# Optimization experiments

Hardware: AMD Instinct MI355X
Metric: run time of the kernel (lower is better)

The kernel has to match this reference:

```python
import jax, jax.numpy as jnp
import numpy as np

B, S, HID = 4, 2048, 1024
NH, IM, E = 4, 2048, 4
EPS = 1e-6


def setup_inputs() -> dict:
    key = jax.random.key(0)
    ks = jax.random.split(key, 12)
    init = lambda k, shape: (jax.random.normal(k, shape, jnp.float32) * 0.02)
    return {
        "hidden_states": jax.random.normal(ks[0], (B, S, HID), jnp.float32),
        "ln1_w": jnp.ones((HID,), jnp.float32),
        "wq": init(ks[1], (HID, HID)),
        "wk": init(ks[2], (HID, HID)),
        "wv": init(ks[3], (HID, HID)),
        "wo": init(ks[4], (HID, HID)),
        "ln2_w": jnp.ones((HID,), jnp.float32),
        "router_w": init(ks[5], (HID, E)),
        "router_b": jnp.zeros((E,), jnp.float32),
        "gate_w": init(ks[6], (E, HID, IM)),
        "up_w": init(ks[7], (E, HID, IM)),
        "down_w": init(ks[8], (E, IM, HID)),
    }


def _rms(x, w):
    return w * (x * jax.lax.rsqrt(jnp.mean(x * x, axis=-1, keepdims=True) + EPS))


def reference(hidden_states, ln1_w, wq, wk, wv, wo, ln2_w,
              router_w, router_b, gate_w, up_w, down_w):
    b, s, h = hidden_states.shape
    nh, d = NH, h // NH

    # ---- attention block (elu+1 feature map, then full softmax) ----
    x = _rms(hidden_states, ln1_w)
    q = (x @ wq).reshape(b, s, nh, d).transpose(0, 2, 1, 3)  # [b,nh,s,d]
    k = (x @ wk).reshape(b, s, nh, d).transpose(0, 2, 1, 3)
    v = (x @ wv).reshape(b, s, nh, d).transpose(0, 2, 1, 3)
    q = jax.nn.elu(q) + 1.0
    k = jax.nn.elu(k) + 1.0
    scores = jnp.einsum('bhqd,bhkd->bhqk', q, k)
    attn = jax.nn.softmax(scores, axis=-1)  # dropout is identity at eval
    o = jnp.einsum('bhqk,bhkd->bhqd', attn, v)
    o = o.transpose(0, 2, 1, 3).reshape(b, s, h) @ wo
    h1 = hidden_states + o

    # ---- MoE block: router softmax, balance loss, dense expert loop ----
    x2 = _rms(h1, ln2_w)
    logits = x2 @ router_w + router_b            # [b,s,E]
    rw = jax.nn.softmax(logits, axis=-1)
    mean_routing = rw.mean(axis=0)               # mean over batch dim only, [s,E]
    balance_loss = jnp.mean((mean_routing - 1.0 / E) ** 2) * 0.01

    # source computes EVERY expert over all tokens, weighted by the FULL
    # softmax routing weight (top-k weights are computed but unused)
    moe_out = jnp.zeros_like(x2)
    for i in range(E):
        g = jax.nn.silu(x2 @ gate_w[i])
        u = x2 @ up_w[i]
        moe_out = moe_out + ((g * u) @ down_w[i]) * rw[..., i:i + 1]

    return h1 + moe_out, balance_loss
```

## Files before the change

### kernel.cpp

```cpp
#include <hip/hip_runtime.h>
#include <cstdint>
#include <cstddef>

#define B_    4
#define S_    2048
#define HID_  1024
#define NH_   4
#define HD_   256
#define IM_   2048
#define E_    4
#define M_    8192
#define NHG_  4

typedef __bf16 bf16x8 __attribute__((ext_vector_type(8)));
typedef float  f32x4  __attribute__((ext_vector_type(4)));

__device__ __forceinline__ unsigned short f32_to_bf16(float f) {
  unsigned int u = __float_as_uint(f);
  u += 0x7fffu + ((u >> 16) & 1u);
  return (unsigned short)(u >> 16);
}

__device__ __forceinline__ void gload16(const unsigned short* g, unsigned short* l) {
  __builtin_amdgcn_global_load_lds(
      (const __attribute__((address_space(1))) void*)g,
      (__attribute__((address_space(3))) void*)l, 16, 0, 0);
}

__device__ __forceinline__ void swizzle_xy(int& bx, int& by) {
  const int gx = gridDim.x, gy = gridDim.y;
  const int flat = blockIdx.x + blockIdx.y * gx;
  const int xcd = flat & 7, i = flat >> 3;
  const int rpx = gy >> 3;
  bx = i % gx;
  by = xcd * rpx + i / gx;
}

#define EPI_F32      0
#define EPI_VT       2
#define EPI_PV_O     3
#define EPI_WO       4
#define EPI_DOWN     5

struct EpiAux {
  float* c_f32;
  unsigned short* c_bf16;
  const float* add_src;
  float* out2;
  long long strideCz;
  int ldc;
};

template<int EPI>
__global__ __launch_bounds__(256) void gemm_bf16k(
    const unsigned short* __restrict__ A, int lda, long long sAo, long long sAi, int zbA,
    const unsigned short* __restrict__ B, int ldb, long long sBo, long long sBi, int zbB,
    int zshift, int zmask, int zbC, int K, EpiAux aux)
{
  __shared__ unsigned short As[2][128 * 32];
  __shared__ unsigned short Bs[2][128 * 32];

  const int t = threadIdx.x;
  int bx, by;
  swizzle_xy(bx, by);
  const int m0 = by * 128, n0 = bx * 128;
  const int z  = blockIdx.z;
  const int zA = z + zbA, zB = z + zbB, zC = z + zbC;
  const unsigned short* Ab = A + (long long)(zA >> zshift) * sAo + (long long)(zA & zmask) * sAi;
  const unsigned short* Bb = B + (long long)(zB >> zshift) * sBo + (long long)(zB & zmask) * sBi;

  const int lane = t & 63, wave = t >> 6;
  const int wm = (wave >> 1) * 64, wn = (wave & 1) * 64;
  const int lrow = lane & 15, quad = lane >> 4;

  f32x4 acc[4][4] = {};

  const int srow = lane >> 2;
  const int sko  = (lane & 3) * 8;
  const unsigned short* aRow0 = Ab + (long long)(m0 + wave * 16       + srow) * lda + sko;
  const unsigned short* aRow1 = Ab + (long long)(m0 + (wave + 4) * 16 + srow) * lda + sko;
  const unsigned short* bRow0 = Bb + (long long)(n0 + wave * 16       + srow) * ldb + sko;
  const unsigned short* bRow1 = Bb + (long long)(n0 + (wave + 4) * 16 + srow) * ldb + sko;
  const int dst0 = (wave * 16) * 32, dst1 = ((wave + 4) * 16) * 32;

  gload16(aRow0, &As[0][dst0]);
  gload16(aRow1, &As[0][dst1]);
  gload16(bRow0, &Bs[0][dst0]);
  gload16(bRow1, &Bs[0][dst1]);

  int cur = 0;
  for (int kk = 0; kk < K; kk += 32, cur ^= 1) {
    __syncthreads();
    if (kk + 32 < K) {
      const int nxt = cur ^ 1, k2 = kk + 32;
      gload16(aRow0 + k2, &As[nxt][dst0]);
      gload16(aRow1 + k2, &As[nxt][dst1]);
      gload16(bRow0 + k2, &Bs[nxt][dst0]);
      gload16(bRow1 + k2, &Bs[nxt][dst1]);
    }
    bf16x8 af[4], bfr[4];
    #pragma unroll
    for (int i = 0; i < 4; ++i) {
      af[i]  = *reinterpret_cast<const bf16x8*>(&As[cur][(wm + i * 16 + lrow) * 32 + quad * 8]);
      bfr[i] = *reinterpret_cast<const bf16x8*>(&Bs[cur][(wn + i * 16 + lrow) * 32 + quad * 8]);
    }
    #pragma unroll
    for (int i = 0; i < 4; ++i)
      #pragma unroll
      for (int j = 0; j < 4; ++j)
        acc[i][j] = __builtin_amdgcn_mfma_f32_16x16x32_bf16(af[i], bfr[j], acc[i][j], 0, 0, 0);
  }

  #pragma unroll
  for (int mi = 0; mi < 4; ++mi) {
    #pragma unroll
    for (int ni = 0; ni < 4; ++ni) {
      #pragma unroll
      for (int r = 0; r < 4; ++r) {
        const int gm = m0 + wm + mi * 16 + quad * 4 + r;
        const int gn = n0 + wn + ni * 16 + lrow;
        const float val = acc[mi][ni][r];
        if (EPI == EPI_F32) {
          aux.c_f32[(long long)zC * aux.strideCz + (long long)gm * aux.ldc + gn] = val;
        } else if (EPI == EPI_VT) {
          const int b = gm >> 11, s = gm & (S_ - 1);
          const int h = gn >> 8, d = gn & (HD_ - 1);
          aux.c_bf16[((long long)(b * NH_ + h) * HD_ + d) * S_ + s] = f32_to_bf16(val);
        } else if (EPI == EPI_PV_O) {
          const int b = zC >> 2, h = zC & (NH_ - 1);
          aux.c_bf16[((long long)(b * S_ + gm)) * HID_ + h * HD_ + gn] = f32_to_bf16(val);
        } else if (EPI == EPI_WO) {
          const long long idx = (long long)gm * HID_ + gn;
          aux.out2[idx] = val + aux.add_src[idx];
        } else if (EPI == EPI_DOWN) {
          const long long idx = (long long)gm * HID_ + gn;
          aux.out2[idx] += val;
        }
      }
    }
  }
}

#define EPI2_GU 1

template<int EPI2>
__global__ __launch_bounds__(256, 2) void gemm_dual_k(
    const unsigned short* __restrict__ A,
    const unsigned short* __restrict__ B0b,
    const unsigned short* __restrict__ B1b,
    int zb,
    unsigned short* __restrict__ out0, unsigned short* __restrict__ out1,
    const float* __restrict__ rw)
{
  __shared__ unsigned short As[2][128 * 32];
  __shared__ unsigned short B0s[2][128 * 32];
  __shared__ unsigned short B1s[2][128 * 32];

  const int t = threadIdx.x;
  int bx, by;
  swizzle_xy(bx, by);
  const int m0 = by * 128, n0 = bx * 128;

  const int lane = t & 63, wave = t >> 6;
  const int wm = (wave >> 1) * 64, wn = (wave & 1) * 64;
  const int lrow = lane & 15, quad = lane >> 4;

  f32x4 acc0[4][4] = {}, acc1[4][4] = {};

  const int srow = lane >> 2;
  const int sko  = (lane & 3) * 8;
  const unsigned short* aRow0 = A   + (long long)(m0 + wave * 16       + srow) * HID_ + sko;
  const unsigned short* aRow1 = A   + (long long)(m0 + (wave + 4) * 16 + srow) * HID_ + sko;
  const unsigned short* gRow0 = B0b + (long long)(n0 + wave * 16       + srow) * HID_ + sko;
  const unsigned short* gRow1 = B0b + (long long)(n0 + (wave + 4) * 16 + srow) * HID_ + sko;
  const unsigned short* uRow0 = B1b + (long long)(n0 + wave * 16       + srow) * HID_ + sko;
  const unsigned short* uRow1 = B1b + (long long)(n0 + (wave + 4) * 16 + srow) * HID_ + sko;
  const int dst0 = (wave * 16) * 32, dst1 = ((wave + 4) * 16) * 32;

  gload16(aRow0, &As[0][dst0]);
  gload16(aRow1, &As[0][dst1]);
  gload16(gRow0, &B0s[0][dst0]);
  gload16(gRow1, &B0s[0][dst1]);
  gload16(uRow0, &B1s[0][dst0]);
  gload16(uRow1, &B1s[0][dst1]);

  int cur = 0;
  for (int kk = 0; kk < HID_; kk += 32, cur ^= 1) {
    __syncthreads();
    if (kk + 32 < HID_) {
      const int nxt = cur ^ 1, k2 = kk + 32;
      gload16(aRow0 + k2, &As[nxt][dst0]);
      gload16(aRow1 + k2, &As[nxt][dst1]);
      gload16(gRow0 + k2, &B0s[nxt][dst0]);
      gload16(gRow1 + k2, &B0s[nxt][dst1]);
      gload16(uRow0 + k2, &B1s[nxt][dst0]);
      gload16(uRow1 + k2, &B1s[nxt][dst1]);
    }
    bf16x8 af[4], b0[4], b1[4];
    #pragma unroll
    for (int i = 0; i < 4; ++i) {
      af[i] = *reinterpret_cast<const bf16x8*>(&As[cur][(wm + i * 16 + lrow) * 32 + quad * 8]);
      b0[i] = *reinterpret_cast<const bf16x8*>(&B0s[cur][(wn + i * 16 + lrow) * 32 + quad * 8]);
      b1[i] = *reinterpret_cast<const bf16x8*>(&B1s[cur][(wn + i * 16 + lrow) * 32 + quad * 8]);
    }
    #pragma unroll
    for (int i = 0; i < 4; ++i)
      #pragma unroll
      for (int j = 0; j < 4; ++j) {
        acc0[i][j] = __builtin_amdgcn_mfma_f32_16x16x32_bf16(af[i], b0[j], acc0[i][j], 0, 0, 0);
        acc1[i][j] = __builtin_amdgcn_mfma_f32_16x16x32_bf16(af[i], b1[j], acc1[i][j], 0, 0, 0);
      }
  }

  #pragma unroll
  for (int mi = 0; mi < 4; ++mi)
    #pragma unroll
    for (int r = 0; r < 4; ++r) {
      const int gm = m0 + wm + mi * 16 + quad * 4 + r;
      const float rwv = rw[(long long)gm * E_ + zb];
      #pragma unroll
      for (int ni = 0; ni < 4; ++ni) {
        const int gn = n0 + wn + ni * 16 + lrow;
        const float v0 = acc0[mi][ni][r];
        const float v1 = acc1[mi][ni][r];
        const float sg = v0 / (1.f + __expf(-v0));
        out0[(long long)gm * IM_ + gn] = f32_to_bf16(sg * v1 * rwv);
      }
    }
}

#define EPI4_GU   0
#define EPI4_QK   1
#define EPI4_DOWN 2
template<bool DUAL, int EPI, int KTOT, int KROW, bool PAIRK>
__global__ __launch_bounds__(512, 2) void gemm4p_k(
    const unsigned short* A0, const unsigned short* A1,
    const unsigned short* B0b, const unsigned short* B1b,
    const float* __restrict__ rw, int expert,
    unsigned short* out0, unsigned short* out1, float* o_f32)
{
  constexpr int NT  = KTOT / 64;
  constexpr int NT2 = NT / 2;
  __shared__ unsigned short smem[DUAL ? 65536 : 49152];

  const int t = threadIdx.x, wave = t >> 6, lane = t & 63;
  const int lrow = lane & 15, quad = lane >> 4;
  const int wrow0 = (wave >> 1) * 64;
  const int wcol0 = (wave & 1) * 64;

  int bx, by;
  swizzle_xy(bx, by);
  const int m0 = by * 256, n0 = bx * 128;

  const int r8  = lane >> 3;
  const int csw = ((lane & 7) ^ r8) << 4;

  auto stage_unit = [&](const unsigned short* mat, int grow0, int ktl, int ldsElem) {
    #pragma unroll
    for (int i = 0; i < 2; ++i) {
      const char* src = (const char*)(mat + (size_t)(grow0 + wave * 16 + i * 8 + r8) * KROW)
                        + (size_t)ktl * 128 + csw;
      gload16((const unsigned short*)src, &smem[ldsElem + wave * 1024 + i * 512]);
    }
  };
  auto stageA = [&](int kt, int buf) {
    const unsigned short* m = A0; int ktl = kt;
    if (PAIRK && kt >= NT2) { m = A1; ktl = kt - NT2; }
    stage_unit(m, m0,       ktl, buf * 16384);
    stage_unit(m, m0 + 128, ktl, buf * 16384 + 8192);
  };
  auto stageB = [&](int kt, int buf, int which) {
    const unsigned short* m; int ktl = kt; int base;
    if (PAIRK) {
      if (kt >= NT2) { m = B1b; ktl = kt - NT2; } else { m = B0b; }
      base = 32768;
    } else {
      m = which ? B1b : B0b;
      base = which ? 49152 : 32768;
    }
    stage_unit(m, n0, ktl, base + buf * 8192);
  };

  const int xr = (lane & 7) << 4;
  auto readA_ = [&](bf16x8* o, int buf, int ks) {
    const char* base = (const char*)smem + buf * 32768 + (wrow0 >> 7) * 16384;
    const int rl0 = wrow0 & 64;
    #pragma unroll
    for (int mi = 0; mi < 4; ++mi)
      o[mi] = *(const bf16x8*)(base + (rl0 + mi * 16 + lrow) * 128 + ((ks * 64 + quad * 16) ^ xr));
  };
  auto readB_ = [&](bf16x8* o, int buf, int which, int ks) {
    const char* base = (const char*)smem + (which ? 98304 : 65536) + buf * 16384;
    #pragma unroll
    for (int nj = 0; nj < 4; ++nj)
      o[nj] = *(const bf16x8*)(base + (wcol0 + nj * 16 + lrow) * 128 + ((ks * 64 + quad * 16) ^ xr));
  };

  f32x4 acc0[4][4] = {};
  f32x4 acc1[4][4] = {};
  auto mm = [&](f32x4 (&ac)[4][4], const bf16x8* aF, const bf16x8* bF) {
    #pragma unroll
    for (int mi = 0; mi < 4; ++mi)
      #pragma unroll
      for (int nj = 0; nj < 4; ++nj)
        ac[mi][nj] = __builtin_amdgcn_mfma_f32_16x16x32_bf16(aF[mi], bF[nj], ac[mi][nj], 0, 0, 0);
  };

  stageA(0, 0);
  stageB(0, 0, 0);
  if (DUAL) stageB(0, 0, 1);
  stageA(1, 1);
  asm volatile("s_waitcnt vmcnt(4)" ::: "memory");
  __builtin_amdgcn_s_barrier();

  bf16x8 a0[4], a1[4], bF[4];
  for (int T = 0; T < NT; ++T) {
    const int c = T & 1;
    if (DUAL) {
      readA_(a0, c, 0); readB_(bF, c, 0, 0);
      if (T + 1 < NT) stageB(T + 1, c ^ 1, 0);
      __builtin_amdgcn_s_barrier();
      asm volatile("s_waitcnt lgkmcnt(0)" ::: "memory");
      __builtin_amdgcn_s_setprio(1); mm(acc0, a0, bF); __builtin_amdgcn_s_setprio(0);
      __builtin_amdgcn_s_barrier();
      readB_(bF, c, 1, 0);
      if (T + 1 < NT) stageB(T + 1, c ^ 1, 1);
      __builtin_amdgcn_s_barrier();
      asm volatile("s_waitcnt lgkmcnt(0)" ::: "memory");
      __builtin_amdgcn_s_setprio(1); mm(acc1, a0, bF); __builtin_amdgcn_s_setprio(0);
      __builtin_amdgcn_s_barrier();
      readA_(a1, c, 1); readB_(bF, c, 0, 1);
      __builtin_amdgcn_s_barrier();
      asm volatile("s_waitcnt lgkmcnt(0)" ::: "memory");
      __builtin_amdgcn_s_setprio(1); mm(acc0, a1, bF); __builtin_amdgcn_s_setprio(0);
      __builtin_amdgcn_s_barrier();
      readB_(bF, c, 1, 1);
      if (T + 2 < NT) { stageA(T + 2, c); asm volatile("s_waitcnt vmcnt(4)" ::: "memory"); }
      else            { asm volatile("s_waitcnt vmcnt(0)" ::: "memory"); }
      __builtin_amdgcn_s_barrier();
      asm volatile("s_waitcnt lgkmcnt(0)" ::: "memory");
      __builtin_amdgcn_s_setprio(1); mm(acc1, a1, bF); __builtin_amdgcn_s_setprio(0);
      __builtin_amdgcn_s_barrier();
    } else {
      readA_(a0, c, 0); readA_(a1, c, 1); readB_(bF, c, 0, 0);
      if (T + 1 < NT) stageB(T + 1, c ^ 1, 0);
      __builtin_amdgcn_s_barrier();
      asm volatile("s_waitcnt lgkmcnt(0)" ::: "memory");
      __builtin_amdgcn_s_setprio(1); mm(acc0, a0, bF); __builtin_amdgcn_s_setprio(0);
      __builtin_amdgcn_s_barrier();
      readB_(bF, c, 0, 1);
      if (T + 2 < NT) { stageA(T + 2, c); asm volatile("s_waitcnt vmcnt(4)" ::: "memory"); }
      else            { asm volatile("s_waitcnt vmcnt(0)" ::: "memory"); }
      __builtin_amdgcn_s_barrier();
      asm volatile("s_waitcnt lgkmcnt(0)" ::: "memory");
      __builtin_amdgcn_s_setprio(1); mm(acc0, a1, bF); __builtin_amdgcn_s_setprio(0);
      __builtin_amdgcn_s_barrier();
    }
  }

  #pragma unroll
  for (int mi = 0; mi < 4; ++mi) {
    #pragma unroll
    for (int r = 0; r < 4; ++r) {
      const int gm = m0 + wrow0 + mi * 16 + quad * 4 + r;
      float rwv = 0.f;
      if (EPI == EPI4_GU) rwv = rw[(size_t)gm * E_ + expert];
      #pragma unroll
      for (int nj = 0; nj < 4; ++nj) {
        const int gn = n0 + wcol0 + nj * 16 + lrow;
        const float v0 = acc0[mi][nj][r];
        if (EPI == EPI4_GU) {
          const float v1 = acc1[mi][nj][r];
          const float sg = v0 / (1.f + __expf(-v0));
          out0[(size_t)gm * IM_ + gn] = f32_to_bf16(sg * v1 * rwv);
        } else if (EPI == EPI4_QK) {
          const float v1 = acc1[mi][nj][r];
          out0[(size_t)gm * HID_ + gn] = f32_to_bf16(v0 > 0.f ? v0 + 1.f : __expf(v0));
          out1[(size_t)gm * HID_ + gn] = f32_to_bf16(v1 > 0.f ? v1 + 1.f : __expf(v1));
        } else {
          o_f32[(size_t)gm * HID_ + gn] += v0;
        }
      }
    }
  }
}

__global__ void transpose_cast4_k(const float* s0, const float* s1,
                                  const float* s2, const float* s3,
                                  unsigned short* __restrict__ out, int R, int C)
{
  __shared__ float tile[32][33];
  const int z = blockIdx.z;
  const float* in = (z == 0) ? s0 : (z == 1) ? s1 : (z == 2) ? s2 : s3;
  unsigned short* o = out + (long long)z * R * C;
  const int c0 = blockIdx.x * 32, r0 = blockIdx.y * 32;
  const int tx = threadIdx.x, ty = threadIdx.y;
  #pragma unroll
  for (int i = 0; i < 32; i += 8)
    tile[ty + i][tx] = in[(long long)(r0 + ty + i) * C + c0 + tx];
  __syncthreads();
  #pragma unroll
  for (int i = 0; i < 32; i += 8)
    o[(long long)(c0 + ty + i) * R + r0 + tx] = f32_to_bf16(tile[tx][ty + i]);
}

__global__ void transpose_cast2x4_k(const float* __restrict__ sA,
                                    const float* __restrict__ sB,
                                    unsigned short* __restrict__ dA,
                                    unsigned short* __restrict__ dB,
                                    int R, int C)
{
  __shared__ float tile[32][33];
  const int z = blockIdx.z;
  const long long eo = (long long)(z & 3) * R * C;
  const float* in = ((z < 4) ? sA : sB) + eo;
  unsigned short* o = ((z < 4) ? dA : dB) + eo;
  const int c0 = blockIdx.x * 32, r0 = blockIdx.y * 32;
  const int tx = threadIdx.x, ty = threadIdx.y;
  #pragma unroll
  for (int i = 0; i < 32; i += 8)
    tile[ty + i][tx] = in[(long long)(r0 + ty + i) * C + c0 + tx];
  __syncthreads();
  #pragma unroll
  for (int i = 0; i < 32; i += 8)
    o[(long long)(c0 + ty + i) * R + r0 + tx] = f32_to_bf16(tile[tx][ty + i]);
}

__global__ void transpose_cast_k(const float* __restrict__ in,
                                 unsigned short* __restrict__ out, int R, int C)
{
  __shared__ float tile[32][33];
  const long long bo = (long long)blockIdx.z * R * C;
  const int c0 = blockIdx.x * 32, r0 = blockIdx.y * 32;
  const int tx = threadIdx.x, ty = threadIdx.y;
  #pragma unroll
  for (int i = 0; i < 32; i += 8)
    tile[ty + i][tx] = in[bo + (long long)(r0 + ty + i) * C + c0 + tx];
  __syncthreads();
  #pragma unroll
  for (int i = 0; i < 32; i += 8)
    out[bo + (long long)(c0 + ty + i) * R + r0 + tx] = f32_to_bf16(tile[tx][ty + i]);
}

__global__ __launch_bounds__(256) void rmsnorm_cast_k(
    const float* __restrict__ x, const float* __restrict__ w,
    unsigned short* __restrict__ out)
{
  __shared__ float red[4];
  const int row = blockIdx.x, t = threadIdx.x;
  const float4 v = reinterpret_cast<const float4*>(x + (long long)row * HID_)[t];
  float ss = v.x * v.x + v.y * v.y + v.z * v.z + v.w * v.w;
  #pragma unroll
  for (int off = 32; off > 0; off >>= 1) ss += __shfl_down(ss, off, 64);
  if ((t & 63) == 0) red[t >> 6] = ss;
  __syncthreads();
  ss = red[0] + red[1] + red[2] + red[3];
  const float inv = rsqrtf(ss * (1.0f / HID_) + 1e-6f);
  const float4 wv = reinterpret_cast<const float4*>(w)[t];
  ushort4 o;
  o.x = f32_to_bf16(v.x * inv * wv.x);
  o.y = f32_to_bf16(v.y * inv * wv.y);
  o.z = f32_to_bf16(v.z * inv * wv.z);
  o.w = f32_to_bf16(v.w * inv * wv.w);
  reinterpret_cast<ushort4*>(out + (long long)row * HID_)[t] = o;
}

__global__ __launch_bounds__(256) void softmax_rows_k(float* __restrict__ scores)
{
  __shared__ float red[4];
  const long long rbase = ((long long)blockIdx.y * S_ + blockIdx.x) * S_;
  float* row = scores + rbase;
  const int t = threadIdx.x;
  float v[8];
  #pragma unroll
  for (int i = 0; i < 8; ++i) v[i] = row[t + i * 256];
  float m = v[0];
  #pragma unroll
  for (int i = 1; i < 8; ++i) m = fmaxf(m, v[i]);
  #pragma unroll
  for (int off = 32; off > 0; off >>= 1) m = fmaxf(m, __shfl_down(m, off, 64));
  if ((t & 63) == 0) red[t >> 6] = m;
  __syncthreads();
  m = fmaxf(fmaxf(red[0], red[1]), fmaxf(red[2], red[3]));
  __syncthreads();
  float s = 0.f;
  #pragma unroll
  for (int i = 0; i < 8; ++i) { v[i] = __expf(v[i] - m); s += v[i]; }
  #pragma unroll
  for (int off = 32; off > 0; off >>= 1) s += __shfl_down(s, off, 64);
  if ((t & 63) == 0) red[t >> 6] = s;
  __syncthreads();
  const float inv = 1.0f / (red[0] + red[1] + red[2] + red[3]);
  unsigned short* prow = reinterpret_cast<unsigned short*>(scores) + rbase * 2;
  #pragma unroll
  for (int i = 0; i < 8; ++i) prow[t + i * 256] = f32_to_bf16(v[i] * inv);
}

__global__ __launch_bounds__(256) void router_k(
    const float* __restrict__ h1, const float* __restrict__ ln2w,
    const float* __restrict__ rwgt, const float* __restrict__ rbias,
    float* __restrict__ rw)
{
  const int wv = threadIdx.x >> 6, lane = threadIdx.x & 63;
  const long long m = (long long)blockIdx.x * 4 + wv;
  const float* xr = h1 + m * HID_;
  float xv[16];
  float ss = 0.f;
  #pragma unroll
  for (int i = 0; i < 16; ++i) { xv[i] = xr[lane + i * 64]; ss += xv[i] * xv[i]; }
  #pragma unroll
  for (int off = 32; off > 0; off >>= 1) ss += __shfl_down(ss, off, 64);
  ss = __shfl(ss, 0, 64);
  const float inv = rsqrtf(ss * (1.0f / HID_) + 1e-6f);
  float l0 = 0, l1 = 0, l2 = 0, l3 = 0;
  #pragma unroll
  for (int i = 0; i < 16; ++i) {
    const int k = lane + i * 64;
    const float xn = xv[i] * inv * ln2w[k];
    const float4 wr = reinterpret_cast<const float4*>(rwgt)[k];
    l0 += xn * wr.x; l1 += xn * wr.y; l2 += xn * wr.z; l3 += xn * wr.w;
  }
  #pragma unroll
  for (int off = 32; off > 0; off >>= 1) {
    l0 += __shfl_down(l0, off, 64);
    l1 += __shfl_down(l1, off, 64);
    l2 += __shfl_down(l2, off, 64);
    l3 += __shfl_down(l3, off, 64);
  }
  if (lane == 0) {
    l0 += rbias[0]; l1 += rbias[1]; l2 += rbias[2]; l3 += rbias[3];
    const float mx = fmaxf(fmaxf(l0, l1), fmaxf(l2, l3));
    const float e0 = __expf(l0 - mx), e1 = __expf(l1 - mx);
    const float e2 = __expf(l2 - mx), e3 = __expf(l3 - mx);
    const float is = 1.0f / (e0 + e1 + e2 + e3);
    reinterpret_cast<float4*>(rw)[m] = make_float4(e0 * is, e1 * is, e2 * is, e3 * is);
  }
}

__global__ __launch_bounds__(256) void balance_k(const float* __restrict__ rw,
                                                 float* __restrict__ out_scalar)
{
  __shared__ float red[4];
  float acc = 0.f;
  for (int it = threadIdx.x; it < S_ * E_; it += 256) {
    const int s = it >> 2, e = it & 3;
    float mr = 0.f;
    #pragma unroll
    for (int b = 0; b < B_; ++b) mr += rw[((long long)b * S_ + s) * E_ + e];
    mr *= (1.0f / B_);
    const float d = mr - 1.0f / E_;
    acc += d * d;
  }
  #pragma unroll
  for (int off = 32; off > 0; off >>= 1) acc += __shfl_down(acc, off, 64);
  if ((threadIdx.x & 63) == 0) red[threadIdx.x >> 6] = acc;
  __syncthreads();
  if (threadIdx.x == 0)
    out_scalar[0] = (red[0] + red[1] + red[2] + red[3]) * (0.01f / (S_ * E_));
}

extern "C" void kernel_launch(void* const* d_in, const int* in_sizes, int n_in,
                              void* d_out, int out_size, void* d_ws, size_t ws_size,
                              hipStream_t stream)
{
  const float* hidden   = (const float*)d_in[0];
  const float* ln1w     = (const float*)d_in[1];
  const float* wq       = (const float*)d_in[2];
  const float* wk       = (const float*)d_in[3];
  const float* wv       = (const float*)d_in[4];
  const float* wo       = (const float*)d_in[5];
  const float* ln2w     = (const float*)d_in[6];
  const float* router_w = (const float*)d_in[7];
  const float* router_b = (const float*)d_in[8];
  const float* gate_w   = (const float*)d_in[9];
  const float* up_w     = (const float*)d_in[10];
  const float* down_w   = (const float*)d_in[11];
  float* out = (float*)d_out;

  char* ws = (char*)d_ws;
  size_t off = 0;
  auto carve = [&](size_t bytes) {
    off = (off + 255) & ~(size_t)255;
    char* p = ws + off;
    off += bytes;
    return p;
  };
  unsigned short* wqT   = (unsigned short*)carve((size_t)HID_ * HID_ * 2);
  unsigned short* wkT   = (unsigned short*)carve((size_t)HID_ * HID_ * 2);
  unsigned short* wvT   = (unsigned short*)carve((size_t)HID_ * HID_ * 2);
  unsigned short* woT   = (unsigned short*)carve((size_t)HID_ * HID_ * 2);
  unsigned short* x_bf  = (unsigned short*)carve((size_t)M_ * HID_ * 2);
  unsigned short* qb    = (unsigned short*)carve((size_t)M_ * HID_ * 2);
  unsigned short* kb    = (unsigned short*)carve((size_t)M_ * HID_ * 2);
  unsigned short* vT    = (unsigned short*)carve((size_t)M_ * HID_ * 2);
  float*          rwbuf = (float*)carve((size_t)M_ * E_ * 4);
  char*           ubase = carve((size_t)NHG_ * S_ * S_ * 4);
  float*          scores = (float*)ubase;
  unsigned short* gateT = (unsigned short*)(ubase);
  unsigned short* upT   = (unsigned short*)(ubase + (size_t)16 * 1024 * 1024);
  unsigned short* downT = (unsigned short*)(ubase + (size_t)32 * 1024 * 1024);
  unsigned short* o_bf  = x_bf;
  unsigned short* x2_bf = qb;
  unsigned short* gu0   = kb;
  unsigned short* gu1   = (unsigned short*)carve((size_t)M_ * IM_ * 2);
  const bool paired = (ws_size >= off);

  const dim3 blk256(256), blk512(512), blkT(32, 8);

  transpose_cast4_k<<<dim3(32, 32, 4), blkT, 0, stream>>>(wq, wk, wv, wo, wqT, HID_, HID_);

  rmsnorm_cast_k<<<M_, blk256, 0, stream>>>(hidden, ln1w, x_bf);

  gemm4p_k<true, EPI4_QK, 1024, 1024, false><<<dim3(8, 32, 1), blk512, 0, stream>>>(
      x_bf, nullptr, wqT, wkT, nullptr, 0, qb, kb, nullptr);
  {
    EpiAux a{}; a.c_bf16 = vT;
    gemm_bf16k<EPI_VT><<<dim3(8, 64, 1), blk256, 0, stream>>>(
        x_bf, HID_, 0, 0, 0, wvT, HID_, 0, 0, 0, 0, 0, 0, HID_, a);
  }

  for (int grp = 0; grp < 16 / NHG_; ++grp) {
    EpiAux as{}; as.c_f32 = scores; as.ldc = S_; as.strideCz = (long long)S_ * S_;
    gemm_bf16k<EPI_F32><<<dim3(16, 16, NHG_), blk256, 0, stream>>>(
        qb, HID_, (long long)S_ * HID_, HD_, grp * NHG_,
        kb, HID_, (long long)S_ * HID_, HD_, grp * NHG_,
        2, 3, 0, HD_, as);
    softmax_rows_k<<<dim3(S_, NHG_, 1), blk256, 0, stream>>>(scores);
    EpiAux ap{}; ap.c_bf16 = o_bf;
    gemm_bf16k<EPI_PV_O><<<dim3(2, 16, NHG_), blk256, 0, stream>>>(
        (const unsigned short*)scores, 2 * S_, (long long)S_ * 2 * S_, 0, 0,
        vT, S_, (long long)HD_ * S_, 0, grp * NHG_,
        0, 0, grp * NHG_, S_, ap);
  }

  transpose_cast2x4_k<<<dim3(64, 32, 8), blkT, 0, stream>>>(
      gate_w, up_w, gateT, upT, HID_, IM_);
  transpose_cast_k<<<dim3(32, 64, E_), blkT, 0, stream>>>(down_w, downT, IM_, HID_);

  {
    EpiAux a{}; a.add_src = hidden; a.out2 = out;
    gemm_bf16k<EPI_WO><<<dim3(8, 64, 1), blk256, 0, stream>>>(
        o_bf, HID_, 0, 0, 0, woT, HID_, 0, 0, 0, 0, 0, 0, HID_, a);
  }

  rmsnorm_cast_k<<<M_, blk256, 0, stream>>>(out, ln2w, x2_bf);
  router_k<<<M_ / 4, blk256, 0, stream>>>(out, ln2w, router_w, router_b, rwbuf);
  balance_k<<<1, blk256, 0, stream>>>(rwbuf, out + (size_t)M_ * HID_);

  const size_t wsz = (size_t)IM_ * HID_;
  if (paired) {
    for (int p = 0; p < 2; ++p) {
      const int e0 = 2 * p, e1 = e0 + 1;
      gemm4p_k<true, EPI4_GU, 1024, 1024, false><<<dim3(16, 32, 1), blk512, 0, stream>>>(
          x2_bf, nullptr, gateT + (size_t)e0 * wsz, upT + (size_t)e0 * wsz,
          rwbuf, e0, gu0, nullptr, nullptr);
      gemm4p_k<true, EPI4_GU, 1024, 1024, false><<<dim3(16, 32, 1), blk512, 0, stream>>>(
          x2_bf, nullptr, gateT + (size_t)e1 * wsz, upT + (size_t)e1 * wsz,
          rwbuf, e1, gu1, nullptr, nullptr);
      gemm4p_k<false, EPI4_DOWN, 4096, 2048, true><<<dim3(8, 32, 1), blk512, 0, stream>>>(
          gu0, gu1, downT + (size_t)e0 * wsz, downT + (size_t)e1 * wsz,
          nullptr, 0, nullptr, nullptr, out);
    }
  } else {
    for (int i = 0; i < E_; ++i) {
      gemm_dual_k<EPI2_GU><<<dim3(16, 64, 1), blk256, 0, stream>>>(
          x2_bf, gateT + (size_t)i * wsz, upT + (size_t)i * wsz, i, gu0, nullptr, rwbuf);
      EpiAux ad{}; ad.out2 = out;
      gemm_bf16k<EPI_DOWN><<<dim3(8, 64, 1), blk256, 0, stream>>>(
          gu0, IM_, 0, 0, 0, downT + (size_t)i * wsz, IM_, 0, 0, 0,
          0, 0, 0, IM_, ad);
    }
  }
}
```

Measured before the change: 1.070 ms.

## Deepen GEMM prefetch pipeline and route Wo projection through 512-thread GEMM

Restructures the 512-thread GEMM's load schedule. The dual-B path now prefetches the second B matrix two k-tiles ahead. The single-B path gets a three-slot B ring buffer so B is staged two tiles ahead, with vmcnt waits tuned so load latency overlaps more MFMA work. The Wo output projection with residual add moves from the older 256-thread GEMM to this kernel using a new epilogue. Shared memory for the non-dual variant grows, which may affect occupancy, and the hand-counted vmcnt values must stay correct to avoid races.

```diff
diff --git a/kernel.cpp b/kernel.cpp
--- a/kernel.cpp
+++ b/kernel.cpp
@@ -25,6 +25,16 @@
   __builtin_amdgcn_global_load_lds(
       (const __attribute__((address_space(1))) void*)g,
       (__attribute__((address_space(3))) void*)l, 16, 0, 0);
+}
+
+template<int N> __device__ __forceinline__ void vwait() {
+  if constexpr (N == 0)      asm volatile("s_waitcnt vmcnt(0)" ::: "memory");
+  else if constexpr (N == 2) asm volatile("s_waitcnt vmcnt(2)" ::: "memory");
+  else if constexpr (N == 6) asm volatile("s_waitcnt vmcnt(6)" ::: "memory");
+  else                       asm volatile("s_waitcnt vmcnt(8)" ::: "memory");
+}
+__device__ __forceinline__ void lgk0() {
+  asm volatile("s_waitcnt lgkmcnt(0)" ::: "memory");
 }
 
 __device__ __forceinline__ void swizzle_xy(int& bx, int& by) {
@@ -229,19 +239,21 @@
     }
 }
 
-#define EPI4_GU   0
-#define EPI4_QK   1
-#define EPI4_DOWN 2
+#define EPI5_GU   0
+#define EPI5_QK   1
+#define EPI5_DOWN 2
+#define EPI5_WO   3
 template<bool DUAL, int EPI, int KTOT, int KROW, bool PAIRK>
-__global__ __launch_bounds__(512, 2) void gemm4p_k(
+__global__ __launch_bounds__(512, 2) void gemm5_k(
     const unsigned short* A0, const unsigned short* A1,
     const unsigned short* B0b, const unsigned short* B1b,
     const float* __restrict__ rw, int expert,
-    unsigned short* out0, unsigned short* out1, float* o_f32)
+    unsigned short* out0, unsigned short* out1,
+    float* o_f32, const float* add_src)
 {
   constexpr int NT  = KTOT / 64;
   constexpr int NT2 = NT / 2;
-  __shared__ unsigned short smem[DUAL ? 65536 : 49152];
+  __shared__ unsigned short smem[DUAL ? 65536 : 57344];
 
   const int t = threadIdx.x, wave = t >> 6, lane = t & 63;
   const int lrow = lane & 15, quad = lane >> 4;
@@ -255,7 +267,7 @@
   const int r8  = lane >> 3;
   const int csw = ((lane & 7) ^ r8) << 4;
 
-  auto stage_unit = [&](const unsigned short* mat, int grow0, int ktl, int ldsElem) {
+  auto unit = [&](const unsigned short* mat, int grow0, int ktl, int ldsElem) {
     #pragma unroll
     for (int i = 0; i < 2; ++i) {
       const char* src = (const char*)(mat + (size_t)(grow0 + wave * 16 + i * 8 + r8) * KROW)
@@ -263,34 +275,34 @@
       gload16((const unsigned short*)src, &smem[ldsElem + wave * 1024 + i * 512]);
     }
   };
-  auto stageA = [&](int kt, int buf) {
+  auto stageA = [&](int kt) {
     const unsigned short* m = A0; int ktl = kt;
-    if (PAIRK && kt >= NT2) { m = A1; ktl = kt - NT2; }
-    stage_unit(m, m0,       ktl, buf * 16384);
-    stage_unit(m, m0 + 128, ktl, buf * 16384 + 8192);
+    if constexpr (PAIRK) { if (kt >= NT2) { m = A1; ktl = kt - NT2; } }
+    const int buf = kt & 1;
+    unit(m, m0,       ktl, buf * 16384);
+    unit(m, m0 + 128, ktl, buf * 16384 + 8192);
   };
-  auto stageB = [&](int kt, int buf, int which) {
-    const unsigned short* m; int ktl = kt; int base;
-    if (PAIRK) {
-      if (kt >= NT2) { m = B1b; ktl = kt - NT2; } else { m = B0b; }
-      base = 32768;
+  auto stageB = [&](int kt, int which, int bufB) {
+    const unsigned short* m; int ktl = kt;
+    if constexpr (DUAL) {
+      m = which ? B1b : B0b;
     } else {
-      m = which ? B1b : B0b;
-      base = which ? 49152 : 32768;
-    }
-    stage_unit(m, n0, ktl, base + buf * 8192);
+      m = B0b;
+      if constexpr (PAIRK) { if (kt >= NT2) { m = B1b; ktl = kt - NT2; } }
+    }
+    unit(m, n0, ktl, 32768 + (DUAL ? which * 16384 : 0) + bufB * 8192);
   };
 
   const int xr = (lane & 7) << 4;
   auto readA_ = [&](bf16x8* o, int buf, int ks) {
     const char* base = (const char*)smem + buf * 32768 + (wrow0 >> 7) * 16384;
-    const int rl0 = wrow0 & 64;
+    const int rl0 = wrow0 & 127;
     #pragma unroll
     for (int mi = 0; mi < 4; ++mi)
       o[mi] = *(const bf16x8*)(base + (rl0 + mi * 16 + lrow) * 128 + ((ks * 64 + quad * 16) ^ xr));
   };
-  auto readB_ = [&](bf16x8* o, int buf, int which, int ks) {
-    const char* base = (const char*)smem + (which ? 98304 : 65536) + buf * 16384;
+  auto readB_ = [&](bf16x8* o, int baseByte, int ks) {
+    const char* base = (const char*)smem + baseByte;
     #pragma unroll
     for (int nj = 0; nj < 4; ++nj)
       o[nj] = *(const bf16x8*)(base + (wcol0 + nj * 16 + lrow) * 128 + ((ks * 64 + quad * 16) ^ xr));
@@ -306,55 +318,72 @@
         ac[mi][nj] = __builtin_amdgcn_mfma_f32_16x16x32_bf16(aF[mi], bF[nj], ac[mi][nj], 0, 0, 0);
   };
 
-  stageA(0, 0);
-  stageB(0, 0, 0);
-  if (DUAL) stageB(0, 0, 1);
-  stageA(1, 1);
-  asm volatile("s_waitcnt vmcnt(4)" ::: "memory");
-  __builtin_amdgcn_s_barrier();
-
   bf16x8 a0[4], a1[4], bF[4];
-  for (int T = 0; T < NT; ++T) {
-    const int c = T & 1;
-    if (DUAL) {
-      readA_(a0, c, 0); readB_(bF, c, 0, 0);
-      if (T + 1 < NT) stageB(T + 1, c ^ 1, 0);
-      __builtin_amdgcn_s_barrier();
-      asm volatile("s_waitcnt lgkmcnt(0)" ::: "memory");
+
+  if constexpr (DUAL) {
+    stageA(0); stageB(0, 1, 0); stageB(0, 0, 0); stageA(1); stageB(1, 1, 1);
+    vwait<8>();
+    __builtin_amdgcn_s_barrier();
+
+    for (int T = 0; T < NT; ++T) {
+      const int c = T & 1;
+      const int bB1 = 65536 + 32768 + c * 16384;
+      const int bB0 = 65536 + c * 16384;
+      readA_(a0, c, 0);
+      readB_(bF, bB1, 0);
+      if (T + 1 < NT) stageB(T + 1, 0, (T + 1) & 1);
+      if (T < NT - 1) vwait<8>(); else vwait<0>();
+      __builtin_amdgcn_s_barrier();
+      lgk0();
+      __builtin_amdgcn_s_setprio(1); mm(acc1, a0, bF); __builtin_amdgcn_s_setprio(0);
+      __builtin_amdgcn_s_barrier();
+      readB_(bF, bB0, 0);
+      __builtin_amdgcn_s_barrier();
+      lgk0();
       __builtin_amdgcn_s_setprio(1); mm(acc0, a0, bF); __builtin_amdgcn_s_setprio(0);
       __builtin_amdgcn_s_barrier();
-      readB_(bF, c, 1, 0);
-      if (T + 1 < NT) stageB(T + 1, c ^ 1, 1);
-      __builtin_amdgcn_s_barrier();
-      asm volatile("s_waitcnt lgkmcnt(0)" ::: "memory");
-      __builtin_amdgcn_s_setprio(1); mm(acc1, a0, bF); __builtin_amdgcn_s_setprio(0);
-      __builtin_amdgcn_s_barrier();
-      readA_(a1, c, 1); readB_(bF, c, 0, 1);
-      __builtin_amdgcn_s_barrier();
-      asm volatile("s_waitcnt lgkmcnt(0)" ::: "memory");
+      readA_(a1, c, 1);
+      readB_(bF, bB1, 1);
+      __builtin_amdgcn_s_barrier();
+      lgk0();
+      __builtin_amdgcn_s_setprio(1); mm(acc1, a1, bF); __builtin_amdgcn_s_setprio(0);
+      __builtin_amdgcn_s_barrier();
+      readB_(bF, bB0, 1);
+      if (T + 2 < NT) { stageA(T + 2); stageB(T + 2, 1, c); }
+      if (T < NT - 2) vwait<8>();
+      else if (T == NT - 2) vwait<2>();
+      __builtin_amdgcn_s_barrier();
+      lgk0();
       __builtin_amdgcn_s_setprio(1); mm(acc0, a1, bF); __builtin_amdgcn_s_setprio(0);
       __builtin_amdgcn_s_barrier();
-      readB_(bF, c, 1, 1);
-      if (T + 2 < NT) { stageA(T + 2, c); asm volatile("s_waitcnt vmcnt(4)" ::: "memory"); }
-      else            { asm volatile("s_waitcnt vmcnt(0)" ::: "memory"); }
-      __builtin_amdgcn_s_barrier();
-      asm volatile("s_waitcnt lgkmcnt(0)" ::: "memory");
-      __builtin_amdgcn_s_setprio(1); mm(acc1, a1, bF); __builtin_amdgcn_s_setprio(0);
-      __builtin_amdgcn_s_barrier();
-    } else {
-      readA_(a0, c, 0); readA_(a1, c, 1); readB_(bF, c, 0, 0);
-      if (T + 1 < NT) stageB(T + 1, c ^ 1, 0);
-      __builtin_amdgcn_s_barrier();
-      asm volatile("s_waitcnt lgkmcnt(0)" ::: "memory");
+    }
+  } else {
+    stageB(0, 0, 0); stageA(0); stageB(1, 0, 1); stageA(1);
+    vwait<6>();
+    __builtin_amdgcn_s_barrier();
+
+    int b = 0;
+    for (int T = 0; T < NT; ++T) {
+      const int c = T & 1;
+      const int bB = 65536 + b * 16384;
+      int bn = b + 2; if (bn >= 3) bn -= 3;
+      readA_(a0, c, 0);
+      readA_(a1, c, 1);
+      readB_(bF, bB, 0);
+      if (T + 2 < NT) stageB(T + 2, 0, bn);
+      __builtin_amdgcn_s_barrier();
+      lgk0();
       __builtin_amdgcn_s_setprio(1); mm(acc0, a0, bF); __builtin_amdgcn_s_setprio(0);
       __builtin_amdgcn_s_barrier();
-      readB_(bF, c, 0, 1);
-      if (T + 2 < NT) { stageA(T + 2, c); asm volatile("s_waitcnt vmcnt(4)" ::: "memory"); }
-      else            { asm volatile("s_waitcnt vmcnt(0)" ::: "memory"); }
-      __builtin_amdgcn_s_barrier();
-      asm volatile("s_waitcnt lgkmcnt(0)" ::: "memory");
+      readB_(bF, bB, 1);
+      if (T + 2 < NT) stageA(T + 2);
+      if (T < NT - 2) vwait<6>();
+      else if (T == NT - 2) vwait<0>();
+      __builtin_amdgcn_s_barrier();
+      lgk0();
       __builtin_amdgcn_s_setprio(1); mm(acc0, a1, bF); __builtin_amdgcn_s_setprio(0);
       __builtin_amdgcn_s_barrier();
+      if (++b == 3) b = 0;
     }
   }
 
@@ -364,21 +393,24 @@
     for (int r = 0; r < 4; ++r) {
       const int gm = m0 + wrow0 + mi * 16 + quad * 4 + r;
       float rwv = 0.f;
-      if (EPI == EPI4_GU) rwv = rw[(size_t)gm * E_ + expert];
+      if (EPI == EPI5_GU) rwv = rw[(size_t)gm * E_ + expert];
       #pragma unroll
       for (int nj = 0; nj < 4; ++nj) {
         const int gn = n0 + wcol0 + nj * 16 + lrow;
         const float v0 = acc0[mi][nj][r];
-        if (EPI == EPI4_GU) {
+        if (EPI == EPI5_GU) {
           const float v1 = acc1[mi][nj][r];
           const float sg = v0 / (1.f + __expf(-v0));
           out0[(size_t)gm * IM_ + gn] = f32_to_bf16(sg * v1 * rwv);
-        } else if (EPI == EPI4_QK) {
+        } else if (EPI == EPI5_QK) {
           const float v1 = acc1[mi][nj][r];
           out0[(size_t)gm * HID_ + gn] = f32_to_bf16(v0 > 0.f ? v0 + 1.f : __expf(v0));
           out1[(size_t)gm * HID_ + gn] = f32_to_bf16(v1 > 0.f ? v1 + 1.f : __expf(v1));
+        } else if (EPI == EPI5_DOWN) {
+          o_f32[(size_t)gm * HID_ + gn] += v0;
         } else {
-          o_f32[(size_t)gm * HID_ + gn] += v0;
+          const size_t idx = (size_t)gm * HID_ + gn;
+          o_f32[idx] = v0 + add_src[idx];
         }
       }
     }
@@ -611,8 +643,8 @@
 
   rmsnorm_cast_k<<<M_, blk256, 0, stream>>>(hidden, ln1w, x_bf);
 
-  gemm4p_k<true, EPI4_QK, 1024, 1024, false><<<dim3(8, 32, 1), blk512, 0, stream>>>(
-      x_bf, nullptr, wqT, wkT, nullptr, 0, qb, kb, nullptr);
+  gemm5_k<true, EPI5_QK, 1024, 1024, false><<<dim3(8, 32, 1), blk512, 0, stream>>>(
+      x_bf, nullptr, wqT, wkT, nullptr, 0, qb, kb, nullptr, nullptr);
   {
     EpiAux a{}; a.c_bf16 = vT;
     gemm_bf16k<EPI_VT><<<dim3(8, 64, 1), blk256, 0, stream>>>(
@@ -637,11 +669,8 @@
       gate_w, up_w, gateT, upT, HID_, IM_);
   transpose_cast_k<<<dim3(32, 64, E_), blkT, 0, stream>>>(down_w, downT, IM_, HID_);
 
-  {
-    EpiAux a{}; a.add_src = hidden; a.out2 = out;
-    gemm_bf16k<EPI_WO><<<dim3(8, 64, 1), blk256, 0, stream>>>(
-        o_bf, HID_, 0, 0, 0, woT, HID_, 0, 0, 0, 0, 0, 0, HID_, a);
-  }
+  gemm5_k<false, EPI5_WO, 1024, 1024, false><<<dim3(8, 32, 1), blk512, 0, stream>>>(
+      o_bf, nullptr, woT, nullptr, nullptr, 0, nullptr, nullptr, out, hidden);
 
   rmsnorm_cast_k<<<M_, blk256, 0, stream>>>(out, ln2w, x2_bf);
   router_k<<<M_ / 4, blk256, 0, stream>>>(out, ln2w, router_w, router_b, rwbuf);
@@ -651,15 +680,15 @@
   if (paired) {
     for (int p = 0; p < 2; ++p) {
       const int e0 = 2 * p, e1 = e0 + 1;
-      gemm4p_k<true, EPI4_GU, 1024, 1024, false><<<dim3(16, 32, 1), blk512, 0, stream>>>(
+      gemm5_k<true, EPI5_GU, 1024, 1024, false><<<dim3(16, 32, 1), blk512, 0, stream>>>(
           x2_bf, nullptr, gateT + (size_t)e0 * wsz, upT + (size_t)e0 * wsz,
-          rwbuf, e0, gu0, nullptr, nullptr);
-      gemm4p_k<true, EPI4_GU, 1024, 1024, false><<<dim3(16, 32, 1), blk512, 0, stream>>>(
+          rwbuf, e0, gu0, nullptr, nullptr, nullptr);
+      gemm5_k<true, EPI5_GU, 1024, 1024, false><<<dim3(16, 32, 1), blk512, 0, stream>>>(
           x2_bf, nullptr, gateT + (size_t)e1 * wsz, upT + (size_t)e1 * wsz,
-          rwbuf, e1, gu1, nullptr, nullptr);
-      gemm4p_k<false, EPI4_DOWN, 4096, 2048, true><<<dim3(8, 32, 1), blk512, 0, stream>>>(
+          rwbuf, e1, gu1, nullptr, nullptr, nullptr);
+      gemm5_k<false, EPI5_DOWN, 4096, 2048, true><<<dim3(8, 32, 1), blk512, 0, stream>>>(
           gu0, gu1, downT + (size_t)e0 * wsz, downT + (size_t)e1 * wsz,
-          nullptr, 0, nullptr, nullptr, out);
+          nullptr, 0, nullptr, nullptr, out, nullptr);
     }
   } else {
     for (int i = 0; i < E_; ++i) {
```

After: 1.082 ms. About the same (+1.2%).
